# Kernel tuning notes

Hardware: AMD Instinct MI355X
Metric: run time of the kernel (lower is better)

## Reference

```python
import jax, jax.numpy as jnp
import numpy as np

HIDDEN = 1024
NUM_HEADS = 16
HEAD_DIM = HIDDEN // NUM_HEADS


def setup_inputs() -> dict:
    key = jax.random.key(0)
    ks = jax.random.split(key, 9)
    s = 0.02
    return {
        "x": jax.random.normal(ks[0], (2, 2048, HIDDEN), dtype=jnp.float32),
        "wq": jax.random.normal(ks[1], (HIDDEN, HIDDEN), dtype=jnp.float32) * s,
        "bq": jnp.zeros((HIDDEN,), dtype=jnp.float32),
        "wk": jax.random.normal(ks[2], (HIDDEN, HIDDEN), dtype=jnp.float32) * s,
        "bk": jnp.zeros((HIDDEN,), dtype=jnp.float32),
        "wv": jax.random.normal(ks[3], (HIDDEN, HIDDEN), dtype=jnp.float32) * s,
        "bv": jnp.zeros((HIDDEN,), dtype=jnp.float32),
        "wo": jax.random.normal(ks[4], (HIDDEN, HIDDEN), dtype=jnp.float32) * s,
        "bo": jnp.zeros((HIDDEN,), dtype=jnp.float32),
    }


def reference(x, wq, bq, wk, bk, wv, bv, wo, bo):
    B, S, H = x.shape
    # torch nn.Linear: y = x @ W.T + b
    q = x @ wq.T + bq
    k = x @ wk.T + bk
    v = x @ wv.T + bv
    # [B, S, nH, dH] -> [B, nH, S, dH]
    q = q.reshape(B, S, NUM_HEADS, HEAD_DIM).transpose(0, 2, 1, 3)
    k = k.reshape(B, S, NUM_HEADS, HEAD_DIM).transpose(0, 2, 1, 3)
    v = v.reshape(B, S, NUM_HEADS, HEAD_DIM).transpose(0, 2, 1, 3)
    scores = jnp.einsum("bhqd,bhkd->bhqk", q, k)
    probs = jax.nn.softmax(scores / jnp.sqrt(jnp.float32(HEAD_DIM)), axis=-1)
    context = jnp.einsum("bhqk,bhkd->bhqd", probs, v)
    context = context.transpose(0, 2, 1, 3).reshape(B, S, H)
    return context @ wo.T + bo
```

## Files before the change

kernel.cpp:

```cpp
#include <hip/hip_runtime.h>
#include <hip/hip_bf16.h>
#include <math.h>

#define HID   1024
#define NHEAD 16
#define DHEAD 64
#define BATCH 2
#define SEQ   2048
#define TOK   (BATCH*SEQ)

typedef float f32x4  __attribute__((ext_vector_type(4)));
typedef short short8 __attribute__((ext_vector_type(8)));

__device__ __forceinline__ unsigned short f2bf(float f) {
    unsigned int u = __float_as_uint(f);
    u += 0x7FFFu + ((u >> 16) & 1u);
    return (unsigned short)(u >> 16);
}

__device__ __forceinline__ unsigned pk2(float lo, float hi) {
    union { __hip_bfloat162 h; unsigned u; } cv;
    cv.h = __float22bfloat162_rn(make_float2(lo, hi));
    return cv.u;
}

__device__ __forceinline__ void gll16(const unsigned short* g, unsigned short* l) {
    __builtin_amdgcn_global_load_lds(
        (const __attribute__((address_space(1))) void*)g,
        (__attribute__((address_space(3))) void*)l, 16, 0, 0);
}

__global__ __launch_bounds__(256) void cvt_bf16(const float* __restrict__ in,
                                                unsigned short* __restrict__ out, int n8) {
    int i = blockIdx.x * 256 + threadIdx.x;
    if (i >= n8) return;
    const float4* p = (const float4*)in;
    float4 a = p[2*i], b = p[2*i+1];
    uint4 r;
    r.x = pk2(a.x, a.y); r.y = pk2(a.z, a.w);
    r.z = pk2(b.x, b.y); r.w = pk2(b.z, b.w);
    ((uint4*)out)[i] = r;
}

__global__ __launch_bounds__(256) void cvt_bf16_w4(
    const float* __restrict__ i0, const float* __restrict__ i1,
    const float* __restrict__ i2, const float* __restrict__ i3,
    unsigned short* __restrict__ o0, unsigned short* __restrict__ o1,
    unsigned short* __restrict__ o2, unsigned short* __restrict__ o3, int n8) {
    int i = blockIdx.x * 256 + threadIdx.x;
    if (i >= n8) return;
    int z = blockIdx.y;
    const float* in = (z==0)?i0:((z==1)?i1:((z==2)?i2:i3));
    unsigned short* out = (z==0)?o0:((z==1)?o1:((z==2)?o2:o3));
    const float4* p = (const float4*)in;
    float4 a = p[2*i], b = p[2*i+1];
    uint4 r;
    r.x = pk2(a.x, a.y); r.y = pk2(a.z, a.w);
    r.z = pk2(b.x, b.y); r.w = pk2(b.z, b.w);
    ((uint4*)out)[i] = r;
}

template<int NZ, bool OUTF32>
__global__ __launch_bounds__(256, 3) void gemm_gll(
    const unsigned short* __restrict__ A,
    const unsigned short* __restrict__ W0, const unsigned short* __restrict__ W1,
    const unsigned short* __restrict__ W2,
    const float* __restrict__ b0, const float* __restrict__ b1, const float* __restrict__ b2,
    void* __restrict__ C0, void* __restrict__ C1, void* __restrict__ C2,
    int M, int N, int K)
{
    __shared__ unsigned short As[128*32];
    __shared__ unsigned short Ws[128*32];

    const unsigned short* W = W0; const float* bias = b0; void* C = C0;
    int z = 0;
    if (NZ > 1) {
        z = blockIdx.z;
        W    = (z==0) ? W0 : ((z==1) ? W1 : W2);
        bias = (z==0) ? b0 : ((z==1) ? b1 : b2);
        C    = (z==0) ? C0 : ((z==1) ? C1 : C2);
    }
    const int tid  = threadIdx.x;
    const int l15  = tid & 15, quad = (tid >> 4) & 3, w = tid >> 6;
    const int wm   = (w >> 1) * 64, wn = (w & 1) * 64;
    const int m0   = blockIdx.y * 128, n0 = blockIdx.x * 128;

    const int lane = tid & 63, w4 = tid >> 6;
    const int grow = lane >> 2;
    const int gchk = (lane & 3) ^ (grow & 3);
    const unsigned short* pa0 = A + (size_t)(m0      + w4*16 + grow) * K + gchk*8;
    const unsigned short* pa1 = A + (size_t)(m0 + 64 + w4*16 + grow) * K + gchk*8;
    const unsigned short* pw0 = W + (size_t)(n0      + w4*16 + grow) * K + gchk*8;
    const unsigned short* pw1 = W + (size_t)(n0 + 64 + w4*16 + grow) * K + gchk*8;
    unsigned short* lA0 = &As[(w4*16)      * 32];
    unsigned short* lA1 = &As[(64 + w4*16) * 32];
    unsigned short* lW0 = &Ws[(w4*16)      * 32];
    unsigned short* lW1 = &Ws[(64 + w4*16) * 32];

    const int rchk = (l15 & 3);

    f32x4 acc[4][4] = {};

    for (int k0 = 0; k0 < K; k0 += 32) {
        gll16(pa0, lA0); gll16(pa1, lA1);
        gll16(pw0, lW0); gll16(pw1, lW1);
        pa0 += 32; pa1 += 32; pw0 += 32; pw1 += 32;
        __syncthreads();

        short8 af[4], bfv[4];
        const int co = (quad ^ rchk) * 8;
        #pragma unroll
        for (int mi = 0; mi < 4; ++mi) af[mi]  = *(const short8*)&As[(wm + mi*16 + l15)*32 + co];
        #pragma unroll
        for (int ni = 0; ni < 4; ++ni) bfv[ni] = *(const short8*)&Ws[(wn + ni*16 + l15)*32 + co];
        #pragma unroll
        for (int mi = 0; mi < 4; ++mi)
            #pragma unroll
            for (int ni = 0; ni < 4; ++ni)
                acc[mi][ni] = __builtin_amdgcn_mfma_f32_16x16x32_bf16(af[mi], bfv[ni], acc[mi][ni], 0, 0, 0);
        __syncthreads();
    }

    float bv[4];
    #pragma unroll
    for (int ni = 0; ni < 4; ++ni) bv[ni] = bias[n0 + wn + ni*16 + l15];

    if (NZ == 3 && z == 2) {
        #pragma unroll
        for (int mi = 0; mi < 4; ++mi)
            #pragma unroll
            for (int ni = 0; ni < 4; ++ni) {
                const int row0 = m0 + wm + mi*16 + quad*4;
                const int col  = n0 + wn + ni*16 + l15;
                const int hh = col >> 6, dd = col & 63;
                const int bb = row0 >> 11, ss = row0 & 2047;
                ushort4 r4;
                r4.x = f2bf(acc[mi][ni][0] + bv[ni]);
                r4.y = f2bf(acc[mi][ni][1] + bv[ni]);
                r4.z = f2bf(acc[mi][ni][2] + bv[ni]);
                r4.w = f2bf(acc[mi][ni][3] + bv[ni]);
                *(ushort4*)((unsigned short*)C + ((size_t)(bb*NHEAD + hh)*DHEAD + dd)*SEQ + ss) = r4;
            }
    } else {
        #pragma unroll
        for (int mi = 0; mi < 4; ++mi)
            #pragma unroll
            for (int ni = 0; ni < 4; ++ni)
                #pragma unroll
                for (int r = 0; r < 4; ++r) {
                    const int row = m0 + wm + mi*16 + quad*4 + r;
                    const int col = n0 + wn + ni*16 + l15;
                    const float val = acc[mi][ni][r] + bv[ni];
                    if (OUTF32) ((float*)C)[(size_t)row*N + col] = val;
                    else ((unsigned short*)C)[(size_t)row*N + col] = f2bf(val);
                }
    }
}

__global__ __launch_bounds__(256, 2) void attn_v4(
    const unsigned short* __restrict__ Qg, const unsigned short* __restrict__ Kg,
    const unsigned short* __restrict__ vT,
    unsigned short* __restrict__ pO0, unsigned short* __restrict__ pO1,
    float* __restrict__ pl)
{
    __shared__ unsigned short Ks[2][64][64];
    __shared__ unsigned short VT[2][64][64];
    __shared__ unsigned short PTs[4*64*64];

    const int tid  = threadIdx.x;
    const int l15  = tid & 15, quad = (tid >> 4) & 3, w = tid >> 6;
    const int z    = blockIdx.z;
    const int b    = z & 1, half = z >> 1;
    const int h    = blockIdx.y;
    const int q0   = blockIdx.x * 256;
    const size_t rowbase = (size_t)b * SEQ;
    const int    cbase   = h * DHEAD;
    const size_t vbase   = (size_t)(b*NHEAD + h) * DHEAD * SEQ;
    const int    keybase = half * (SEQ/2);

    {
        const unsigned short* src = Qg + (rowbase + q0 + tid) * HID + cbase;
        #pragma unroll
        for (int j = 0; j < 8; ++j)
            *(uint4*)&PTs[tid*64 + ((j ^ (tid & 7)) * 8)] = *(const uint4*)(src + j*8);
    }
    short8 qa[4][2];
    #pragma unroll
    for (int nq = 0; nq < 4; ++nq)
        #pragma unroll
        for (int s2 = 0; s2 < 2; ++s2)
            qa[nq][s2] = *(const short8*)&PTs[(w*64 + nq*16 + l15)*64 + (((s2*4 + quad) ^ (l15 & 7)) * 8)];

    const int sr = tid >> 2, sc = (tid & 3) * 16;
    const int c0 = (sc >> 3) ^ (sr & 7);
    const int c1 = ((sc >> 3) + 1) ^ (sr & 7);
    {
        const unsigned short* ks = Kg + (rowbase + keybase + sr) * HID + cbase + sc;
        const unsigned short* vs = vT + vbase + (size_t)sr * SEQ + keybase + sc;
        *(uint4*)&Ks[0][sr][c0*8] = *(const uint4*)ks;
        *(uint4*)&Ks[0][sr][c1*8] = *(const uint4*)(ks + 8);
        *(uint4*)&VT[0][sr][c0*8] = *(const uint4*)vs;
        *(uint4*)&VT[0][sr][c1*8] = *(const uint4*)(vs + 8);
    }

    f32x4 o[4][4] = {};
    float lsum[4] = {0.f, 0.f, 0.f, 0.f};
    unsigned short* myPT = &PTs[w*64*64];

    for (int kt = 0; kt < SEQ/2/64; ++kt) {
        const int buf = kt & 1;
        __syncthreads();

        uint4 kr0, kr1, vr0, vr1;
        const bool pre = (kt + 1 < SEQ/2/64);
        if (pre) {
            const unsigned short* ks = Kg + (rowbase + keybase + (kt+1)*64 + sr) * HID + cbase + sc;
            const unsigned short* vs = vT + vbase + (size_t)sr * SEQ + keybase + (kt+1)*64 + sc;
            kr0 = *(const uint4*)ks; kr1 = *(const uint4*)(ks + 8);
            vr0 = *(const uint4*)vs; vr1 = *(const uint4*)(vs + 8);
        }

        f32x4 s[4][4] = {};
        #pragma unroll
        for (int s2 = 0; s2 < 2; ++s2) {
            short8 kfr[4];
            #pragma unroll
            for (int mi = 0; mi < 4; ++mi)
                kfr[mi] = *(const short8*)&Ks[buf][mi*16 + l15][((s2*4 + quad) ^ (l15 & 7)) * 8];
            #pragma unroll
            for (int mi = 0; mi < 4; ++mi)
                #pragma unroll
                for (int nq = 0; nq < 4; ++nq)
                    s[mi][nq] = __builtin_amdgcn_mfma_f32_16x16x32_bf16(kfr[mi], qa[nq][s2], s[mi][nq], 0, 0, 0);
        }

        #pragma unroll
        for (int mi = 0; mi < 4; ++mi)
            #pragma unroll
            for (int nq = 0; nq < 4; ++nq) {
                const float p0 = __expf(s[mi][nq][0] * 0.125f);
                const float p1 = __expf(s[mi][nq][1] * 0.125f);
                const float p2 = __expf(s[mi][nq][2] * 0.125f);
                const float p3 = __expf(s[mi][nq][3] * 0.125f);
                lsum[nq] += (p0 + p1) + (p2 + p3);
                uint2 u; u.x = pk2(p0, p1); u.y = pk2(p2, p3);
                const int off = (((2*mi + (quad >> 1)) ^ (l15 & 7)) * 8) + (quad & 1) * 4;
                *(uint2*)&myPT[(nq*16 + l15)*64 + off] = u;
            }

        #pragma unroll
        for (int ks2 = 0; ks2 < 2; ++ks2) {
            short8 ptb[4], vfr[4];
            #pragma unroll
            for (int nq = 0; nq < 4; ++nq)
                ptb[nq] = *(const short8*)&myPT[(nq*16 + l15)*64 + ((ks2*4 + quad) ^ (l15 & 7)) * 8];
            #pragma unroll
            for (int md = 0; md < 4; ++md)
                vfr[md] = *(const short8*)&VT[buf][md*16 + l15][((ks2*4 + quad) ^ (l15 & 7)) * 8];
            #pragma unroll
            for (int md = 0; md < 4; ++md)
                #pragma unroll
                for (int nq = 0; nq < 4; ++nq)
                    o[md][nq] = __builtin_amdgcn_mfma_f32_16x16x32_bf16(vfr[md], ptb[nq], o[md][nq], 0, 0, 0);
        }

        if (pre) {
            const int nb = buf ^ 1;
            *(uint4*)&Ks[nb][sr][c0*8] = kr0;
            *(uint4*)&Ks[nb][sr][c1*8] = kr1;
            *(uint4*)&VT[nb][sr][c0*8] = vr0;
            *(uint4*)&VT[nb][sr][c1*8] = vr1;
        }
    }

    unsigned short* pO = half ? pO1 : pO0;
    #pragma unroll
    for (int nq = 0; nq < 4; ++nq) {
        float l = lsum[nq];
        l += __shfl_xor(l, 16);
        l += __shfl_xor(l, 32);
        if (quad == 0)
            pl[(((size_t)half * BATCH + b) * NHEAD + h) * SEQ + q0 + w*64 + nq*16 + l15] = l;
        const size_t row = rowbase + q0 + w*64 + nq*16 + l15;
        #pragma unroll
        for (int md = 0; md < 4; ++md) {
            ushort4 u;
            u.x = f2bf(o[md][nq][0]); u.y = f2bf(o[md][nq][1]);
            u.z = f2bf(o[md][nq][2]); u.w = f2bf(o[md][nq][3]);
            *(ushort4*)&pO[row * HID + cbase + md*16 + quad*4] = u;
        }
    }
}

__device__ __forceinline__ unsigned addpair(unsigned a, unsigned c, float inv) {
    float a0 = __uint_as_float(a << 16), a1 = __uint_as_float(a & 0xffff0000u);
    float c0 = __uint_as_float(c << 16), c1 = __uint_as_float(c & 0xffff0000u);
    return pk2((a0 + c0) * inv, (a1 + c1) * inv);
}

__global__ __launch_bounds__(256) void reduce_ctx(
    const unsigned short* __restrict__ p0, const unsigned short* __restrict__ p1,
    const float* __restrict__ pl, unsigned short* __restrict__ ctx)
{
    const int i  = blockIdx.x * 256 + threadIdx.x;
    const int e0 = i * 8;
    const int t  = e0 >> 10;
    const int h  = (e0 & 1023) >> 6;
    const int b  = t >> 11, q = t & 2047;
    const float l0 = pl[(((size_t)0 * BATCH + b) * NHEAD + h) * SEQ + q];
    const float l1 = pl[(((size_t)1 * BATCH + b) * NHEAD + h) * SEQ + q];
    const float inv = 1.f / (l0 + l1);
    uint4 a = ((const uint4*)p0)[i];
    uint4 c = ((const uint4*)p1)[i];
    uint4 r;
    r.x = addpair(a.x, c.x, inv);
    r.y = addpair(a.y, c.y, inv);
    r.z = addpair(a.z, c.z, inv);
    r.w = addpair(a.w, c.w, inv);
    ((uint4*)ctx)[i] = r;
}

extern "C" void kernel_launch(void* const* d_in, const int* in_sizes, int n_in,
                              void* d_out, int out_size, void* d_ws, size_t ws_size,
                              hipStream_t stream)
{
    const float* x  = (const float*)d_in[0];
    const float* wq = (const float*)d_in[1];
    const float* bq = (const float*)d_in[2];
    const float* wk = (const float*)d_in[3];
    const float* bk = (const float*)d_in[4];
    const float* wv = (const float*)d_in[5];
    const float* bv = (const float*)d_in[6];
    const float* wo = (const float*)d_in[7];
    const float* bo = (const float*)d_in[8];
    float* out = (float*)d_out;

    unsigned short* xb  = (unsigned short*)d_ws;
    unsigned short* wqb = xb  + (size_t)TOK * HID;
    unsigned short* wkb = wqb + (size_t)HID * HID;
    unsigned short* wvb = wkb + (size_t)HID * HID;
    unsigned short* wob = wvb + (size_t)HID * HID;
    unsigned short* qb  = wob + (size_t)HID * HID;
    unsigned short* kb  = qb  + (size_t)TOK * HID;
    unsigned short* vtb = kb  + (size_t)TOK * HID;
    unsigned short* cb  = vtb + (size_t)TOK * HID;

    const dim3 blk(256);
    cvt_bf16<<<dim3(TOK*HID/8/256), blk, 0, stream>>>(x, xb, TOK*HID/8);
    cvt_bf16_w4<<<dim3(HID*HID/8/256, 4), blk, 0, stream>>>(
        wq, wk, wv, wo, wqb, wkb, wvb, wob, HID*HID/8);

    gemm_gll<3, false><<<dim3(HID/128, TOK/128, 3), blk, 0, stream>>>(
        xb, wqb, wkb, wvb, bq, bk, bv, qb, kb, vtb, TOK, HID, HID);

    attn_v4<<<dim3(SEQ/256, NHEAD, 4), blk, 0, stream>>>(
        qb, kb, vtb, cb, xb, (float*)wqb);

    reduce_ctx<<<dim3(TOK*HID/8/256), blk, 0, stream>>>(cb, xb, (float*)wqb, qb);

    gemm_gll<1, true><<<dim3(HID/128, TOK/128, 1), blk, 0, stream>>>(
        qb, wob, wob, wob, bo, bo, bo, out, out, out, TOK, HID, HID);
}
```

Baseline: 210.0 us.

## Fold softmax scale into Q weights, use exp2, and template GEMM tile sizes

Pre-multiplies the Q weights and bias by log2(e)/8 during conversion so the attention kernel can call a native exp2 directly instead of scaling and calling __expf. The GEMM is templated on tile shape: the QKV projection moves to 256x128 tiles at 2 waves per SIMD, and the output projection to 128x64 tiles at 4 waves. This cuts per-element multiplies in the softmax and rebalances GEMM grid size against per-block data reuse. Larger QKV tiles raise register and LDS pressure, and scaling Q before rounding to bf16 changes rounding slightly.

```diff
diff --git a/kernel.cpp b/kernel.cpp
--- a/kernel.cpp
+++ b/kernel.cpp
@@ -9,6 +9,8 @@
 #define SEQ   2048
 #define TOK   (BATCH*SEQ)
 
+#define LOG2E_8 0.18033688011112042f
+
 typedef float f32x4  __attribute__((ext_vector_type(4)));
 typedef short short8 __attribute__((ext_vector_type(8)));
 
@@ -22,6 +24,14 @@
     union { __hip_bfloat162 h; unsigned u; } cv;
     cv.h = __float22bfloat162_rn(make_float2(lo, hi));
     return cv.u;
+}
+
+__device__ __forceinline__ float fexp2(float x) {
+#if __has_builtin(__builtin_amdgcn_exp2f)
+    return __builtin_amdgcn_exp2f(x);
+#else
+    return __expf(x * 0.6931471805599453f);
+#endif
 }
 
 __device__ __forceinline__ void gll16(const unsigned short* g, unsigned short* l) {
@@ -52,16 +62,17 @@
     int z = blockIdx.y;
     const float* in = (z==0)?i0:((z==1)?i1:((z==2)?i2:i3));
     unsigned short* out = (z==0)?o0:((z==1)?o1:((z==2)?o2:o3));
+    const float s = (z == 0) ? LOG2E_8 : 1.0f;
     const float4* p = (const float4*)in;
     float4 a = p[2*i], b = p[2*i+1];
     uint4 r;
-    r.x = pk2(a.x, a.y); r.y = pk2(a.z, a.w);
-    r.z = pk2(b.x, b.y); r.w = pk2(b.z, b.w);
+    r.x = pk2(a.x*s, a.y*s); r.y = pk2(a.z*s, a.w*s);
+    r.z = pk2(b.x*s, b.y*s); r.w = pk2(b.z*s, b.w*s);
     ((uint4*)out)[i] = r;
 }
 
-template<int NZ, bool OUTF32>
-__global__ __launch_bounds__(256, 3) void gemm_gll(
+template<int BM, int BN, int NZ, bool OUTF32, int MINW>
+__global__ __launch_bounds__(256, MINW) void gemm_t(
     const unsigned short* __restrict__ A,
     const unsigned short* __restrict__ W0, const unsigned short* __restrict__ W1,
     const unsigned short* __restrict__ W2,
@@ -69,8 +80,13 @@
     void* __restrict__ C0, void* __restrict__ C1, void* __restrict__ C2,
     int M, int N, int K)
 {
-    __shared__ unsigned short As[128*32];
-    __shared__ unsigned short Ws[128*32];
+    constexpr int MT = BM/32;
+    constexpr int NT = BN/32;
+    constexpr int AG = BM/64;
+    constexpr int WG = BN/64;
+
+    __shared__ unsigned short As[BM*32];
+    __shared__ unsigned short Ws[BN*32];
 
     const unsigned short* W = W0; const float* bias = b0; void* C = C0;
     int z = 0;
@@ -82,54 +98,61 @@
     }
     const int tid  = threadIdx.x;
     const int l15  = tid & 15, quad = (tid >> 4) & 3, w = tid >> 6;
-    const int wm   = (w >> 1) * 64, wn = (w & 1) * 64;
-    const int m0   = blockIdx.y * 128, n0 = blockIdx.x * 128;
-
-    const int lane = tid & 63, w4 = tid >> 6;
+    const int wm   = (w >> 1) * (BM/2), wn = (w & 1) * (BN/2);
+    const int m0   = blockIdx.y * BM, n0 = blockIdx.x * BN;
+
+    const int lane = tid & 63;
     const int grow = lane >> 2;
     const int gchk = (lane & 3) ^ (grow & 3);
-    const unsigned short* pa0 = A + (size_t)(m0      + w4*16 + grow) * K + gchk*8;
-    const unsigned short* pa1 = A + (size_t)(m0 + 64 + w4*16 + grow) * K + gchk*8;
-    const unsigned short* pw0 = W + (size_t)(n0      + w4*16 + grow) * K + gchk*8;
-    const unsigned short* pw1 = W + (size_t)(n0 + 64 + w4*16 + grow) * K + gchk*8;
-    unsigned short* lA0 = &As[(w4*16)      * 32];
-    unsigned short* lA1 = &As[(64 + w4*16) * 32];
-    unsigned short* lW0 = &Ws[(w4*16)      * 32];
-    unsigned short* lW1 = &Ws[(64 + w4*16) * 32];
-
-    const int rchk = (l15 & 3);
-
-    f32x4 acc[4][4] = {};
+
+    const unsigned short* pA[AG]; unsigned short* lA[AG];
+    const unsigned short* pW[WG]; unsigned short* lW[WG];
+    #pragma unroll
+    for (int i = 0; i < AG; ++i) {
+        const int r = w*(BM/4) + i*16;
+        pA[i] = A + (size_t)(m0 + r + grow) * K + gchk*8;
+        lA[i] = &As[r * 32];
+    }
+    #pragma unroll
+    for (int i = 0; i < WG; ++i) {
+        const int r = w*(BN/4) + i*16;
+        pW[i] = W + (size_t)(n0 + r + grow) * K + gchk*8;
+        lW[i] = &Ws[r * 32];
+    }
+
+    f32x4 acc[MT][NT] = {};
 
     for (int k0 = 0; k0 < K; k0 += 32) {
-        gll16(pa0, lA0); gll16(pa1, lA1);
-        gll16(pw0, lW0); gll16(pw1, lW1);
-        pa0 += 32; pa1 += 32; pw0 += 32; pw1 += 32;
+        #pragma unroll
+        for (int i = 0; i < AG; ++i) { gll16(pA[i], lA[i]); pA[i] += 32; }
+        #pragma unroll
+        for (int i = 0; i < WG; ++i) { gll16(pW[i], lW[i]); pW[i] += 32; }
         __syncthreads();
 
-        short8 af[4], bfv[4];
-        const int co = (quad ^ rchk) * 8;
-        #pragma unroll
-        for (int mi = 0; mi < 4; ++mi) af[mi]  = *(const short8*)&As[(wm + mi*16 + l15)*32 + co];
-        #pragma unroll
-        for (int ni = 0; ni < 4; ++ni) bfv[ni] = *(const short8*)&Ws[(wn + ni*16 + l15)*32 + co];
-        #pragma unroll
-        for (int mi = 0; mi < 4; ++mi)
-            #pragma unroll
-            for (int ni = 0; ni < 4; ++ni)
+        const int co = (quad ^ (l15 & 3)) * 8;
+        short8 af[MT], bfv[NT];
+        #pragma unroll
+        for (int mi = 0; mi < MT; ++mi) af[mi]  = *(const short8*)&As[(wm + mi*16 + l15)*32 + co];
+        #pragma unroll
+        for (int ni = 0; ni < NT; ++ni) bfv[ni] = *(const short8*)&Ws[(wn + ni*16 + l15)*32 + co];
+        #pragma unroll
+        for (int mi = 0; mi < MT; ++mi)
+            #pragma unroll
+            for (int ni = 0; ni < NT; ++ni)
                 acc[mi][ni] = __builtin_amdgcn_mfma_f32_16x16x32_bf16(af[mi], bfv[ni], acc[mi][ni], 0, 0, 0);
         __syncthreads();
     }
 
-    float bv[4];
-    #pragma unroll
-    for (int ni = 0; ni < 4; ++ni) bv[ni] = bias[n0 + wn + ni*16 + l15];
+    const float bsc = (NZ == 3 && z == 0) ? LOG2E_8 : 1.0f;
+    float bv[NT];
+    #pragma unroll
+    for (int ni = 0; ni < NT; ++ni) bv[ni] = bias[n0 + wn + ni*16 + l15] * bsc;
 
     if (NZ == 3 && z == 2) {
         #pragma unroll
-        for (int mi = 0; mi < 4; ++mi)
-            #pragma unroll
-            for (int ni = 0; ni < 4; ++ni) {
+        for (int mi = 0; mi < MT; ++mi)
+            #pragma unroll
+            for (int ni = 0; ni < NT; ++ni) {
                 const int row0 = m0 + wm + mi*16 + quad*4;
                 const int col  = n0 + wn + ni*16 + l15;
                 const int hh = col >> 6, dd = col & 63;
@@ -143,9 +166,9 @@
             }
     } else {
         #pragma unroll
-        for (int mi = 0; mi < 4; ++mi)
-            #pragma unroll
-            for (int ni = 0; ni < 4; ++ni)
+        for (int mi = 0; mi < MT; ++mi)
+            #pragma unroll
+            for (int ni = 0; ni < NT; ++ni)
                 #pragma unroll
                 for (int r = 0; r < 4; ++r) {
                     const int row = m0 + wm + mi*16 + quad*4 + r;
@@ -157,7 +180,7 @@
     }
 }
 
-__global__ __launch_bounds__(256, 2) void attn_v4(
+__global__ __launch_bounds__(256, 2) void attn_v5(
     const unsigned short* __restrict__ Qg, const unsigned short* __restrict__ Kg,
     const unsigned short* __restrict__ vT,
     unsigned short* __restrict__ pO0, unsigned short* __restrict__ pO1,
@@ -238,10 +261,10 @@
         for (int mi = 0; mi < 4; ++mi)
             #pragma unroll
             for (int nq = 0; nq < 4; ++nq) {
-                const float p0 = __expf(s[mi][nq][0] * 0.125f);
-                const float p1 = __expf(s[mi][nq][1] * 0.125f);
-                const float p2 = __expf(s[mi][nq][2] * 0.125f);
-                const float p3 = __expf(s[mi][nq][3] * 0.125f);
+                const float p0 = fexp2(s[mi][nq][0]);
+                const float p1 = fexp2(s[mi][nq][1]);
+                const float p2 = fexp2(s[mi][nq][2]);
+                const float p3 = fexp2(s[mi][nq][3]);
                 lsum[nq] += (p0 + p1) + (p2 + p3);
                 uint2 u; u.x = pk2(p0, p1); u.y = pk2(p2, p3);
                 const int off = (((2*mi + (quad >> 1)) ^ (l15 & 7)) * 8) + (quad & 1) * 4;
@@ -350,14 +373,14 @@
     cvt_bf16_w4<<<dim3(HID*HID/8/256, 4), blk, 0, stream>>>(
         wq, wk, wv, wo, wqb, wkb, wvb, wob, HID*HID/8);
 
-    gemm_gll<3, false><<<dim3(HID/128, TOK/128, 3), blk, 0, stream>>>(
+    gemm_t<256, 128, 3, false, 2><<<dim3(HID/128, TOK/256, 3), blk, 0, stream>>>(
         xb, wqb, wkb, wvb, bq, bk, bv, qb, kb, vtb, TOK, HID, HID);
 
-    attn_v4<<<dim3(SEQ/256, NHEAD, 4), blk, 0, stream>>>(
+    attn_v5<<<dim3(SEQ/256, NHEAD, 4), blk, 0, stream>>>(
         qb, kb, vtb, cb, xb, (float*)wqb);
 
     reduce_ctx<<<dim3(TOK*HID/8/256), blk, 0, stream>>>(cb, xb, (float*)wqb, qb);
 
-    gemm_gll<1, true><<<dim3(HID/128, TOK/128, 1), blk, 0, stream>>>(
+    gemm_t<128, 64, 1, true, 4><<<dim3(HID/64, TOK/128, 1), blk, 0, stream>>>(
         qb, wob, wob, wob, bo, bo, bo, out, out, out, TOK, HID, HID);
 }
```

After: 211.2 us. Within noise of the previous version (+0.6%).
